# Kernel tuning notes

Hardware: AMD Instinct MI355X
Metric: run time of the kernel (lower is better)

## Reference

```python
import jax, jax.numpy as jnp
import numpy as np

RADII = (3, 5, 7)      # window_levels
S, B, D = 1024, 8, 512  # seq_len, batch, feature_dim
EPS = 1e-12             # F.normalize eps


def setup_inputs() -> dict:
    key = jax.random.key(0)
    k0, k1, k2 = jax.random.split(key, 3)
    x = jax.random.normal(k0, (S, B, D), jnp.float32)          # seq-first like the torch path
    W = jax.random.normal(k1, (3, D, D), jnp.float32) / np.sqrt(D)  # 3 level linear weights
    b = jax.random.normal(k2, (3, D), jnp.float32) * 0.01           # 3 level linear biases
    alphas = jnp.ones((3,), jnp.float32)   # nn.Parameter(torch.ones)
    betas = jnp.zeros((3,), jnp.float32)   # nn.Parameter(torch.zeros)
    return {"x": x, "W": W, "b": b, "alphas": alphas, "betas": betas}


def reference(x, W, b, alphas, betas):
    # x: [S, B, D] (seq-first). torch code transposes to [B, S, D], works, transposes back.
    # Dropout is identity (eval mode). output = x + sum over levels of per-timestep
    # windowed, similarity-weighted sums of linearly transformed neighbors; all
    # windows read the ORIGINAL x, so levels are independent additive terms.
    xb = jnp.transpose(x, (1, 0, 2))  # [B, S, D]
    Bn, Sn, Dn = xb.shape
    dt = xb.dtype
    # L2-normalized features (F.normalize with eps=1e-12)
    xnorm = xb / jnp.maximum(jnp.linalg.norm(xb, axis=-1, keepdims=True), EPS)
    # prefix sums for O(1) window means (edge-truncated windows)
    csum = jnp.concatenate([jnp.zeros((Bn, 1, Dn), dt), jnp.cumsum(xb, axis=1)], axis=1)
    t_idx = jnp.arange(Sn)
    out = xb
    for m, r in enumerate(RADII):
        starts = jnp.clip(t_idx - r, 0, Sn)        # [S]
        ends = jnp.clip(t_idx + r + 1, 0, Sn)      # [S]
        cnt = (ends - starts).astype(dt)           # window sizes (truncated at edges)
        center = (csum[:, ends, :] - csum[:, starts, :]) / cnt[None, :, None]  # [B,S,D]
        cnorm = center / jnp.maximum(jnp.linalg.norm(center, axis=-1, keepdims=True), EPS)
        # sliding-window gather indices, masked at sequence edges
        offs = jnp.arange(-r, r + 1)
        pos = t_idx[:, None] + offs[None, :]       # [S, w]
        valid = ((pos >= 0) & (pos < Sn)).astype(dt)
        idx = jnp.clip(pos, 0, Sn - 1)
        nw = xnorm[:, idx, :]                      # [B, S, w, D]
        sim = jnp.einsum('bswd,bsd->bsw', nw, cnorm)  # cosine similarity to window mean
        wts = jax.nn.sigmoid(alphas[m] * sim + betas[m]) * valid[None, :, :]
        tfm = xb @ W[m].T + b[m]                   # level-m linear transform, computed once
        tw = tfm[:, idx, :]                        # [B, S, w, D]
        out = out + jnp.einsum('bsw,bswd->bsd', wts, tw)
    return jnp.transpose(out, (1, 0, 2))  # back to [S, B, D]
```

## Files before the change

kernel.cpp:

```cpp
#include <hip/hip_runtime.h>

typedef __attribute__((ext_vector_type(8))) short short8;
typedef __attribute__((ext_vector_type(4))) float f32x4;

#define S_LEN 1024
#define B_N 8
#define D_DIM 512
#define SLAB 4194304
#define NX   4194304

static __device__ __forceinline__ unsigned short f2bf(float f){
  unsigned int u = __float_as_uint(f);
  u = u + 0x7fffu + ((u>>16)&1u);
  return (unsigned short)(u>>16);
}
static __device__ __forceinline__ float bf2f(unsigned short h){
  return __uint_as_float(((unsigned int)h)<<16);
}
static __device__ __forceinline__ ushort4 cvt4(float4 v){
  ushort4 h; h.x=f2bf(v.x); h.y=f2bf(v.y); h.z=f2bf(v.z); h.w=f2bf(v.w); return h;
}

#define GLL16(g,l) __builtin_amdgcn_global_load_lds( \
    (__attribute__((address_space(1))) void*)(g), \
    (__attribute__((address_space(3))) void*)(l), 16, 0, 0)

#define SBAR() do { __builtin_amdgcn_sched_barrier(0); \
  asm volatile("s_barrier" ::: "memory"); \
  __builtin_amdgcn_sched_barrier(0); } while(0)
#define VMCNT(n) asm volatile("s_waitcnt vmcnt(" #n ")" ::: "memory")

__global__ __launch_bounds__(256) void k_conv(const float* __restrict__ x,
    const float* __restrict__ W, unsigned short* __restrict__ xbf,
    unsigned short* __restrict__ wbf)
{
  int tid = blockIdx.x*256 + threadIdx.x;
  const float4* xs = (const float4*)x;
  ushort4* xd = (ushort4*)xbf;
  float4 v0 = xs[tid];
  float4 v1 = xs[tid + 262144];
  float4 v2 = xs[tid + 524288];
  float4 v3 = xs[tid + 786432];
  xd[tid         ] = cvt4(v0);
  xd[tid + 262144] = cvt4(v1);
  xd[tid + 524288] = cvt4(v2);
  xd[tid + 786432] = cvt4(v3);
  if (tid < 196608){
    const float4* ws_ = (const float4*)W;
    ushort4* wd = (ushort4*)wbf;
    wd[tid] = cvt4(ws_[tid]);
  }
}

__global__ __launch_bounds__(256) void k_heavy(const unsigned short* __restrict__ A,
    const unsigned short* __restrict__ Bw, const float* __restrict__ bias,
    unsigned short* __restrict__ C, float* __restrict__ Gband)
{
  __shared__ __align__(16) unsigned short smem[24576];
  int blk = blockIdx.x;
  int tid = threadIdx.x, lane = tid & 63, w = tid >> 6;

  if (blk >= 768){
    int g = blk - 768;
    int b = g & 7, i0 = (g >> 3) * 16;
    #pragma unroll
    for (int q = 0; q < 12; ++q){
      int r = w*12 + q;
      int t = i0 - 16 + r;
      t = t < 0 ? 0 : (t > S_LEN-1 ? S_LEN-1 : t);
      const unsigned short* src = A + ((size_t)(t*B_N + b))*512 + ((lane ^ (r & 7))*8);
      GLL16(src, smem + r*512);
    }
    __syncthreads();
    int j0 = i0 + (w - 1) * 16;
    if (w < 3 && j0 >= 0 && j0 < S_LEN){
      int l15 = lane & 15;
      int cbase = lane >> 4;
      int sw = l15 & 7;
      f32x4 acc = (f32x4){0.f,0.f,0.f,0.f};
      #pragma unroll
      for (int kt = 0; kt < 16; ++kt){
        int ch = (kt*4 + cbase) ^ sw;
        short8 af = *(const short8*)(smem + (16 + l15)*512 + ch*8);
        short8 bf = *(const short8*)(smem + (w*16 + l15)*512 + ch*8);
        acc = __builtin_amdgcn_mfma_f32_16x16x32_bf16(af, bf, acc, 0,0,0);
      }
      int rb = (lane >> 4) * 4;
      #pragma unroll
      for (int rg = 0; rg < 4; ++rg){
        int i = i0 + rb + rg;
        int dl = j0 + l15 - i;
        if (dl >= -14 && dl <= 14)
          Gband[((size_t)b * S_LEN + i) * 32 + dl + 14] = acc[rg];
      }
    }
    return;
  }

  int xcd = blk & 7, ixc = blk >> 3;
  int by = xcd * 8 + ixc / 12;
  int bx = ixc % 12;
  int wm = w >> 1, wn = w & 1;
  int c0 = w*128 + lane, c1 = c0 + 64;
  const unsigned short* gA0 = A + (size_t)(by*128 + (c0>>2))*512 + (c0&3)*8;
  const unsigned short* gA1 = A + (size_t)(by*128 + (c1>>2))*512 + (c1&3)*8;
  const unsigned short* gB0 = Bw + (size_t)(bx*128 + (c0>>2))*512 + (c0&3)*8;
  const unsigned short* gB1 = Bw + (size_t)(bx*128 + (c1>>2))*512 + (c1&3)*8;
  f32x4 acc[4][4];
  #pragma unroll
  for (int i=0;i<4;++i)
    #pragma unroll
    for (int j=0;j<4;++j)
      acc[i][j] = (f32x4){0.f,0.f,0.f,0.f};
  int l15 = lane & 15, klo = (lane>>4)*8;
  {
    unsigned short* s0 = smem + w*1024;
    GLL16(gA0, s0); GLL16(gA1, s0 + 512);
    GLL16(gB0, s0 + 4096); GLL16(gB1, s0 + 4096 + 512);
    gA0 += 32; gA1 += 32; gB0 += 32; gB1 += 32;
    unsigned short* s1 = smem + 8192 + w*1024;
    GLL16(gA0, s1); GLL16(gA1, s1 + 512);
    GLL16(gB0, s1 + 4096); GLL16(gB1, s1 + 4096 + 512);
    gA0 += 32; gA1 += 32; gB0 += 32; gB1 += 32;
  }
  VMCNT(4); SBAR();
  #pragma unroll
  for (int kt = 0; kt < 16; ++kt){
    unsigned short* sc = smem + (kt % 3)*8192;
    if (kt + 2 < 16){
      unsigned short* sn = smem + ((kt + 2) % 3)*8192 + w*1024;
      GLL16(gA0, sn); GLL16(gA1, sn + 512);
      GLL16(gB0, sn + 4096); GLL16(gB1, sn + 4096 + 512);
      gA0 += 32; gA1 += 32; gB0 += 32; gB1 += 32;
    }
    short8 af[4], bfr[4];
    #pragma unroll
    for (int i=0;i<4;++i)
      af[i] = *(const short8*)(sc + (wm*64 + i*16 + l15)*32 + klo);
    #pragma unroll
    for (int j=0;j<4;++j)
      bfr[j] = *(const short8*)(sc + 4096 + (wn*64 + j*16 + l15)*32 + klo);
    #pragma unroll
    for (int i=0;i<4;++i)
      #pragma unroll
      for (int j=0;j<4;++j)
        acc[i][j] = __builtin_amdgcn_mfma_f32_16x16x32_bf16(af[i], bfr[j], acc[i][j], 0,0,0);
    if (kt < 15){
      __builtin_amdgcn_sched_barrier(0);
      if (kt + 2 < 16){ VMCNT(4); }
      else            { VMCNT(0); }
      SBAR();
    }
  }
  __syncthreads();
  int rbase = (lane>>4)*4;
  #pragma unroll
  for (int j=0;j<4;++j){
    int nl = wn*64 + j*16 + l15;
    float bv = bias[bx*128 + nl];
    #pragma unroll
    for (int i=0;i<4;++i){
      int rl0 = wm*64 + i*16 + rbase;
      #pragma unroll
      for (int rg=0;rg<4;++rg)
        smem[(rl0+rg)*128 + nl] = f2bf(acc[i][j][rg] + bv);
    }
  }
  __syncthreads();
  int m_r = bx >> 2, colb = (bx&3)*128;
  #pragma unroll
  for (int p=0;p<8;++p){
    int R = p*16 + (tid>>4);
    int ch = (tid&15)*8;
    uint4 v = *(const uint4*)(smem + R*128 + ch);
    *(uint4*)(C + (size_t)m_r*SLAB + (size_t)(by*128 + R)*512 + colb + ch) = v;
  }
}

__global__ __launch_bounds__(128) void k_gath(const float* __restrict__ x,
    const unsigned short* __restrict__ tfm, const float* __restrict__ Gband,
    const float* __restrict__ alphas, const float* __restrict__ betas,
    float* __restrict__ out)
{
  int blk = blockIdx.x;
  int b = blk & 7, t = blk >> 3;
  int j = threadIdx.x;
  int d0 = j * 4;
  size_t xoff = ((size_t)t * B_N + b) * D_DIM + d0;
  float4 a = *(const float4*)(x + xoff);
  uint2 tv[33];
  #pragma unroll
  for (int p = 0; p < 33; ++p){
    int pm, pr, wsl;
    if (p < 7){ pm = 0; pr = 3; wsl = p; }
    else if (p < 18){ pm = 1; pr = 5; wsl = p - 7; }
    else { pm = 2; pr = 7; wsl = p - 18; }
    int ppos = t + wsl - pr;
    if (ppos >= 0 && ppos < S_LEN)
      tv[p] = *(const uint2*)(tfm + (size_t)pm * SLAB + ((size_t)ppos * B_N + b) * D_DIM + d0);
    else
      tv[p] = make_uint2(0u, 0u);
  }
  __shared__ float pshare[33];
  __shared__ float invc[3];
  __shared__ float wsh[33];
  int m = 0, pos = 0, valid = 0;
  float pp = 0.f, invnp = 0.f;
  if (j < 33){
    int r, wsl;
    if (j < 7){ m = 0; r = 3; wsl = j; }
    else if (j < 18){ m = 1; r = 5; wsl = j - 7; }
    else { m = 2; r = 7; wsl = j - 18; }
    pos = t + wsl - r;
    valid = (pos >= 0 && pos < S_LEN);
    if (valid){
      const float* grow = Gband + ((size_t)b * S_LEN + pos) * 32;
      int ulo = max(t - r, 0), uhi = min(t + r, S_LEN - 1);
      for (int uu = ulo; uu <= uhi; ++uu) pp += grow[uu - pos + 14];
      invnp = rsqrtf(fmaxf(grow[14], 1e-24f));
    }
    pshare[j] = valid ? pp : 0.f;
  }
  __syncthreads();
  if (j < 3){
    int s0 = j == 0 ? 0 : (j == 1 ? 7 : 18);
    int c  = j == 0 ? 7 : (j == 1 ? 11 : 15);
    float s = 0.f;
    for (int k = 0; k < c; ++k) s += pshare[s0 + k];
    invc[j] = rsqrtf(fmaxf(s, 1e-24f));
  }
  __syncthreads();
  if (j < 33){
    float wt = 0.f;
    if (valid){
      float sim = pp * invnp * invc[m];
      float z = alphas[m] * sim + betas[m];
      wt = 1.0f / (1.0f + expf(-z));
    }
    wsh[j] = wt;
  }
  __syncthreads();
  float ax = a.x, ay = a.y, az = a.z, aw = a.w;
  #pragma unroll
  for (int p = 0; p < 33; ++p){
    float wt = wsh[p];
    uint2 uv = tv[p];
    ax += wt * bf2f((unsigned short)(uv.x & 0xffffu));
    ay += wt * bf2f((unsigned short)(uv.x >> 16));
    az += wt * bf2f((unsigned short)(uv.y & 0xffffu));
    aw += wt * bf2f((unsigned short)(uv.y >> 16));
  }
  *(float4*)(out + xoff) = make_float4(ax, ay, az, aw);
}

extern "C" void kernel_launch(void* const* d_in, const int* in_sizes, int n_in,
                              void* d_out, int out_size, void* d_ws, size_t ws_size,
                              hipStream_t stream) {
  const float* x      = (const float*)d_in[0];
  const float* W      = (const float*)d_in[1];
  const float* bias   = (const float*)d_in[2];
  const float* alphas = (const float*)d_in[3];
  const float* betas  = (const float*)d_in[4];
  float* out = (float*)d_out;
  char* ws = (char*)d_ws;
  unsigned short* xbf  = (unsigned short*)ws;
  unsigned short* wbf  = (unsigned short*)(ws + 8388608);
  unsigned short* tfm  = (unsigned short*)(ws + 8388608 + 1572864);
  float*          Gband= (float*)(ws + 8388608 + 1572864 + 25165824);

  k_conv <<<1024, 256, 0, stream>>>(x, W, xbf, wbf);
  k_heavy<<<1280, 256, 0, stream>>>(xbf, wbf, bias, tfm, Gband);
  k_gath <<<8192, 128, 0, stream>>>(x, tfm, Gband, alphas, betas, out);
}
```

Measured before the change: 59.76 us.

## Fuse banded Gram computation into bf16 conversion pre-pass

```diff
diff --git a/kernel.cpp b/kernel.cpp
--- a/kernel.cpp
+++ b/kernel.cpp
@@ -7,7 +7,6 @@
 #define B_N 8
 #define D_DIM 512
 #define SLAB 4194304
-#define NX   4194304
 
 static __device__ __forceinline__ unsigned short f2bf(float f){
   unsigned int u = __float_as_uint(f);
@@ -30,73 +29,86 @@
   __builtin_amdgcn_sched_barrier(0); } while(0)
 #define VMCNT(n) asm volatile("s_waitcnt vmcnt(" #n ")" ::: "memory")
 
-__global__ __launch_bounds__(256) void k_conv(const float* __restrict__ x,
+__global__ __launch_bounds__(256) void k_pre(const float* __restrict__ x,
     const float* __restrict__ W, unsigned short* __restrict__ xbf,
-    unsigned short* __restrict__ wbf)
+    unsigned short* __restrict__ wbf, float* __restrict__ Gband)
 {
-  int tid = blockIdx.x*256 + threadIdx.x;
-  const float4* xs = (const float4*)x;
-  ushort4* xd = (ushort4*)xbf;
-  float4 v0 = xs[tid];
-  float4 v1 = xs[tid + 262144];
-  float4 v2 = xs[tid + 524288];
-  float4 v3 = xs[tid + 786432];
-  xd[tid         ] = cvt4(v0);
-  xd[tid + 262144] = cvt4(v1);
-  xd[tid + 524288] = cvt4(v2);
-  xd[tid + 786432] = cvt4(v3);
-  if (tid < 196608){
+  __shared__ __align__(16) unsigned short smem[24576];
+  int blk = blockIdx.x;
+  int tid = threadIdx.x;
+  if (blk >= 512){
+    int base = (blk - 512)*1024 + tid;
     const float4* ws_ = (const float4*)W;
     ushort4* wd = (ushort4*)wbf;
-    wd[tid] = cvt4(ws_[tid]);
+    #pragma unroll
+    for (int q = 0; q < 4; ++q){
+      int i = base + q*256;
+      wd[i] = cvt4(ws_[i]);
+    }
+    return;
+  }
+  int b = blk & 7, i0 = (blk >> 3) * 16;
+  int lane = tid & 63, w = tid >> 6;
+  #pragma unroll
+  for (int q = 0; q < 12; ++q){
+    int c = q*256 + tid;
+    int row = c >> 6, k = c & 63;
+    int gk = k ^ (row & 7);
+    int t = i0 - 16 + row;
+    t = t < 0 ? 0 : (t > S_LEN-1 ? S_LEN-1 : t);
+    const float* src = x + ((size_t)(t*B_N + b))*512 + gk*8;
+    float4 lo = *(const float4*)src;
+    float4 hi = *(const float4*)(src + 4);
+    ushort4 a = cvt4(lo), bb = cvt4(hi);
+    uint4 v;
+    v.x = (unsigned int)a.x  | ((unsigned int)a.y  << 16);
+    v.y = (unsigned int)a.z  | ((unsigned int)a.w  << 16);
+    v.z = (unsigned int)bb.x | ((unsigned int)bb.y << 16);
+    v.w = (unsigned int)bb.z | ((unsigned int)bb.w << 16);
+    *(uint4*)(smem + row*512 + k*8) = v;
+  }
+  __syncthreads();
+  #pragma unroll
+  for (int q = 0; q < 4; ++q){
+    int c = q*256 + tid;
+    int row16 = c >> 6, k = c & 63;
+    int row = 16 + row16;
+    int gk = k ^ (row & 7);
+    int trow = i0 + row16;
+    uint4 v = *(const uint4*)(smem + row*512 + k*8);
+    *(uint4*)(xbf + ((size_t)(trow*B_N + b))*512 + gk*8) = v;
+  }
+  int j0 = i0 + (w - 1) * 16;
+  if (w < 3 && j0 >= 0 && j0 < S_LEN){
+    int l15 = lane & 15;
+    int cbase = lane >> 4;
+    int sw = l15 & 7;
+    f32x4 acc = (f32x4){0.f,0.f,0.f,0.f};
+    #pragma unroll
+    for (int kt = 0; kt < 16; ++kt){
+      int ch = (kt*4 + cbase) ^ sw;
+      short8 af = *(const short8*)(smem + (16 + l15)*512 + ch*8);
+      short8 bf = *(const short8*)(smem + (w*16 + l15)*512 + ch*8);
+      acc = __builtin_amdgcn_mfma_f32_16x16x32_bf16(af, bf, acc, 0,0,0);
+    }
+    int rb = (lane >> 4) * 4;
+    #pragma unroll
+    for (int rg = 0; rg < 4; ++rg){
+      int i = i0 + rb + rg;
+      int dl = j0 + l15 - i;
+      if (dl >= -14 && dl <= 14)
+        Gband[((size_t)b * S_LEN + i) * 32 + dl + 14] = acc[rg];
+    }
   }
 }
 
 __global__ __launch_bounds__(256) void k_heavy(const unsigned short* __restrict__ A,
     const unsigned short* __restrict__ Bw, const float* __restrict__ bias,
-    unsigned short* __restrict__ C, float* __restrict__ Gband)
+    unsigned short* __restrict__ C)
 {
   __shared__ __align__(16) unsigned short smem[24576];
   int blk = blockIdx.x;
   int tid = threadIdx.x, lane = tid & 63, w = tid >> 6;
-
-  if (blk >= 768){
-    int g = blk - 768;
-    int b = g & 7, i0 = (g >> 3) * 16;
-    #pragma unroll
-    for (int q = 0; q < 12; ++q){
-      int r = w*12 + q;
-      int t = i0 - 16 + r;
-      t = t < 0 ? 0 : (t > S_LEN-1 ? S_LEN-1 : t);
-      const unsigned short* src = A + ((size_t)(t*B_N + b))*512 + ((lane ^ (r & 7))*8);
-      GLL16(src, smem + r*512);
-    }
-    __syncthreads();
-    int j0 = i0 + (w - 1) * 16;
-    if (w < 3 && j0 >= 0 && j0 < S_LEN){
-      int l15 = lane & 15;
-      int cbase = lane >> 4;
-      int sw = l15 & 7;
-      f32x4 acc = (f32x4){0.f,0.f,0.f,0.f};
-      #pragma unroll
-      for (int kt = 0; kt < 16; ++kt){
-        int ch = (kt*4 + cbase) ^ sw;
-        short8 af = *(const short8*)(smem + (16 + l15)*512 + ch*8);
-        short8 bf = *(const short8*)(smem + (w*16 + l15)*512 + ch*8);
-        acc = __builtin_amdgcn_mfma_f32_16x16x32_bf16(af, bf, acc, 0,0,0);
-      }
-      int rb = (lane >> 4) * 4;
-      #pragma unroll
-      for (int rg = 0; rg < 4; ++rg){
-        int i = i0 + rb + rg;
-        int dl = j0 + l15 - i;
-        if (dl >= -14 && dl <= 14)
-          Gband[((size_t)b * S_LEN + i) * 32 + dl + 14] = acc[rg];
-      }
-    }
-    return;
-  }
-
   int xcd = blk & 7, ixc = blk >> 3;
   int by = xcd * 8 + ixc / 12;
   int bx = ixc % 12;
@@ -268,7 +280,7 @@
   unsigned short* tfm  = (unsigned short*)(ws + 8388608 + 1572864);
   float*          Gband= (float*)(ws + 8388608 + 1572864 + 25165824);
 
-  k_conv <<<1024, 256, 0, stream>>>(x, W, xbf, wbf);
-  k_heavy<<<1280, 256, 0, stream>>>(xbf, wbf, bias, tfm, Gband);
+  k_pre  <<< 704, 256, 0, stream>>>(x, W, xbf, wbf, Gband);
+  k_heavy<<< 768, 256, 0, stream>>>(xbf, wbf, bias, tfm);
   k_gath <<<8192, 128, 0, stream>>>(x, tfm, Gband, alphas, betas, out);
 }
```

Result: no change. 60.07 us (+0.5%).
